# Performance work log

Measured on AMD Instinct MI355X. Metric: run time of the kernel, lower is better.

The kernel has to match this reference:

```python
import jax, jax.numpy as jnp
import numpy as np

N = 10000      # nodes
S = 4          # num_samples (walks per node)
L = 8          # walk length
F_IN = 128     # in_features == out_features (required by SelfSupervise fc)
H = 128        # out_features (GRU hidden)
ORIG = 64      # original_features
SUB = 100      # self-supervision subsample


def _gru(x, h0, Wih, Whh, bih, bhh):
    """Single-layer unidirectional GRU. x: (L, *batch, F); h0: (*batch, H)."""
    def step(hprev, xt):
        gi = xt @ Wih.T + bih            # (*batch, 3H)
        gh = hprev @ Whh.T + bhh
        ir, iz, inn = jnp.split(gi, 3, axis=-1)
        hr, hz, hn = jnp.split(gh, 3, axis=-1)
        r = jax.nn.sigmoid(ir + hr)
        z = jax.nn.sigmoid(iz + hz)
        n = jnp.tanh(inn + r * hn)
        hnew = (1.0 - z) * n + z * hprev
        return hnew, hnew
    hT, ys = jax.lax.scan(step, h0, x)
    return ys, hT                         # ys: (L, *batch, H), hT: (*batch, H)


def setup_inputs() -> dict:
    key = jax.random.key(0)
    ks = jax.random.split(key, 14)
    s = 0.1  # weight scale for numerical sanity
    return {
        "h":     jax.random.normal(ks[0], (N, F_IN), jnp.float32),
        "y0":    jax.random.uniform(ks[1], (N, ORIG), jnp.float32),  # binary-ish targets in [0,1]
        "Wih_w": s * jax.random.normal(ks[2], (3 * H, L), jnp.float32),
        "Whh_w": s * jax.random.normal(ks[3], (3 * H, H), jnp.float32),
        "bih_w": s * jax.random.normal(ks[4], (3 * H,), jnp.float32),
        "bhh_w": s * jax.random.normal(ks[5], (3 * H,), jnp.float32),
        "Wih":   s * jax.random.normal(ks[6], (3 * H, F_IN + H), jnp.float32),
        "Whh":   s * jax.random.normal(ks[7], (3 * H, H), jnp.float32),
        "bih":   s * jax.random.normal(ks[8], (3 * H,), jnp.float32),
        "bhh":   s * jax.random.normal(ks[9], (3 * H,), jnp.float32),
        "W_ss":  s * jax.random.normal(ks[10], (ORIG, F_IN), jnp.float32),
        "b_ss":  s * jax.random.normal(ks[11], (ORIG,), jnp.float32),
        "walks": jax.random.randint(ks[12], (S, N, L), 0, N),
        "idxs":  jax.random.randint(ks[13], (SUB,), 0, N),
    }


def reference(h, y0, Wih_w, Whh_w, bih_w, bhh_w, Wih, Whh, bih, bhh, W_ss, b_ss, walks, idxs):
    # uniqueness: index of first occurrence of each node within its walk, in [0, L)
    uniq = jnp.argmax(walks[..., :, None] == walks[..., None, :], axis=-1)  # (S, N, L)
    walks_f = jnp.flip(walks, axis=-1)
    uniq_f = jnp.flip(uniq, axis=-1)
    u1h = jax.nn.one_hot(uniq_f, L, dtype=h.dtype)          # (S, N, L, L)

    hw = jnp.take(h, walks_f, axis=0)                       # (S, N, L, F_IN) gather

    h0 = jnp.zeros((S, N, H), dtype=h.dtype)
    x_walk = jnp.moveaxis(u1h, -2, 0)                       # (L, S, N, L)
    y_walk, h_walk = _gru(x_walk, h0, Wih_w, Whh_w, bih_w, bhh_w)  # (L,S,N,H), (S,N,H)
    # torch: h_walk.mean(0, keepdim=True) over layer dim of size 1 -> identity

    x_main = jnp.concatenate([jnp.moveaxis(hw, -2, 0), y_walk], axis=-1)  # (L, S, N, F_IN+H)
    y_seq, hT = _gru(x_main, h_walk, Wih, Whh, bih, bhh)    # (L,S,N,H), (S,N,H)
    y = jnp.moveaxis(y_seq, 0, -2)                          # (S, N, L, H)

    # self-supervision: subsample nodes, next-step BCE
    y_t = jnp.take(y0, walks_f, axis=0)[:, idxs, 1:, :]     # (S, SUB, L-1, ORIG)
    y_hat = y[:, idxs, :-1, :] @ W_ss.T + b_ss              # (S, SUB, L-1, ORIG)
    pos_w = 1.0 / jnp.mean(y_t)
    loss = jnp.mean(pos_w * y_t * jax.nn.softplus(-y_hat)
                    + (1.0 - y_t) * jax.nn.softplus(y_hat))

    # torch: h.mean(0) over layer dim of size 1 -> hT; activation = Identity; dropout = eval
    return hT, loss
```

## Files before the change

kernel.cpp:

```cpp
#include <hip/hip_runtime.h>
#include <math.h>

#define NN    10000
#define SSS   4
#define LL    8
#define HH    128
#define NSEQ  40000
#define SUBN  100
#define ORIGF 64
#define MA    48
#define NS    3
#define TA    512

typedef unsigned short u16;
typedef short bf16x8 __attribute__((ext_vector_type(8)));
typedef float f32x4 __attribute__((ext_vector_type(4)));

#define L2E 1.4426950408889634f

#define WL_OFF    0
#define BWRZ_OFF  6144
#define BWIN_OFF  7168
#define BWHN_OFF  7680
#define BMRZ_OFF  8192
#define BMIN_OFF  9216
#define BMHN_OFF  9728
#define HB_OFF    10240
#define HBBUF     2176
#define HB_STR    136
#define HB_SSTR   (2*HBBUF)
#define XB_OFF    36352
#define XB_STR    136
#define XB_SSTR   (128*136)
#define SWF_OFF   140800
#define SUF_OFF   142336
#define SCNT_OFF  143872
#define SANY_OFF  144064
#define LDS_TOTAL 144128

#define WB_BYTE_OFF 64
#define W_HHW_N 49152
#define W_HH_N  49152
#define W_IH_N  98304
#define W_TOTAL (W_HHW_N + W_HH_N + W_IH_N)
#define WS_NEED ((size_t)WB_BYTE_OFF + (size_t)W_TOTAL * 2 + (size_t)NN * HH * 2)

__device__ __forceinline__ float bf2f(u16 u) {
  return __uint_as_float(((unsigned)u) << 16);
}
__device__ __forceinline__ u16 f2bf(float f) {
  unsigned u = __float_as_uint(f);
  u += 0x7fffu + ((u >> 16) & 1u);
  return (u16)(u >> 16);
}
__device__ __forceinline__ bf16x8 pack8(float4 v0, float4 v1) {
  bf16x8 r;
  r[0] = (short)f2bf(v0.x); r[1] = (short)f2bf(v0.y);
  r[2] = (short)f2bf(v0.z); r[3] = (short)f2bf(v0.w);
  r[4] = (short)f2bf(v1.x); r[5] = (short)f2bf(v1.y);
  r[6] = (short)f2bf(v1.z); r[7] = (short)f2bf(v1.w);
  return r;
}
__device__ __forceinline__ float sig2_(float xs) {
  return __builtin_amdgcn_rcpf(1.f + __builtin_amdgcn_exp2f(-xs));
}
__device__ __forceinline__ float tanh2_(float xs) {
  return 1.f - 2.f * __builtin_amdgcn_rcpf(__builtin_amdgcn_exp2f(xs) + 1.f);
}
__device__ __forceinline__ float softplusf_(float x) {
  return fmaxf(x, 0.f) + log1pf(__expf(-fabsf(x)));
}

__global__ void k_zero(float* ws) {
  if (threadIdx.x < 4) ws[threadIdx.x] = 0.f;
}

__global__ void k_prep(const float* __restrict__ whhw, const float* __restrict__ whh,
                       const float* __restrict__ wih, float* __restrict__ ws) {
  const int i = blockIdx.x * 256 + threadIdx.x;
  u16* wb = (u16*)((char*)ws + WB_BYTE_OFF);
  if (i < W_HHW_N) {
    const int row = i >> 7;
    wb[i] = f2bf(whhw[i] * ((row < 256) ? L2E : 2.f * L2E));
  } else if (i < W_HHW_N + W_HH_N) {
    const int j = i - W_HHW_N, row = j >> 7;
    wb[i] = f2bf(whh[j] * ((row < 256) ? L2E : 2.f * L2E));
  } else {
    const int j = i - W_HHW_N - W_HH_N, row = j >> 8;
    wb[i] = f2bf(wih[j] * ((row < 256) ? L2E : 2.f * L2E));
  }
}

__global__ void k_prep_h(const float* __restrict__ h, float* __restrict__ ws) {
  const int i = blockIdx.x * 256 + threadIdx.x;
  u16* hb16 = (u16*)((char*)ws + WB_BYTE_OFF) + W_TOTAL;
  hb16[i] = f2bf(h[i]);
}

template<bool BF>
__global__ __launch_bounds__(TA, 2) void k_rum(
    const float* __restrict__ hfeat, const float* __restrict__ y0,
    const float* __restrict__ WihW,  const float* __restrict__ bihW,
    const float* __restrict__ bhhW,
    const float* __restrict__ bih,   const float* __restrict__ bhh,
    const float* __restrict__ W_ss,  const float* __restrict__ b_ss,
    const int* __restrict__ walks,   const int* __restrict__ idxs,
    float* __restrict__ out, float* __restrict__ ws)
{
  extern __shared__ char sm[];
  u16*   WLb  = (u16*)(sm + WL_OFF);
  float* bwrz = (float*)(sm + BWRZ_OFF);
  float* bwin = (float*)(sm + BWIN_OFF);
  float* bwhn = (float*)(sm + BWHN_OFF);
  float* bmrz = (float*)(sm + BMRZ_OFF);
  float* bmin = (float*)(sm + BMIN_OFF);
  float* bmhn = (float*)(sm + BMHN_OFF);
  u16*   hb   = (u16*)(sm + HB_OFF);
  u16*   xb   = (u16*)(sm + XB_OFF);
  int*   swf  = (int*)(sm + SWF_OFF);
  int*   suf  = (int*)(sm + SUF_OFF);
  int*   scnt = (int*)(sm + SCNT_OFF);
  int*   sany = (int*)(sm + SANY_OFF);

  const u16* wb     = (const u16*)((const char*)ws + WB_BYTE_OFF);
  const u16* whhw_b = wb;
  const u16* whh_b  = wb + W_HHW_N;
  const u16* wih_b  = wb + W_HHW_N + W_HH_N;
  const u16* hf16   = wb + W_TOTAL;

  const int tid = threadIdx.x;
  const int lane = tid & 63, c = lane & 15, qd = lane >> 4;
  const int wv = tid >> 6;
  const int i0 = wv * 16 + c;
  const int q0 = blockIdx.x * MA;

  if (tid < MA) {
    const int m = tid;
    scnt[m] = 0;
    const int q = q0 + m;
    if (q < NSEQ) {
      int w[LL];
      #pragma unroll
      for (int l = 0; l < LL; ++l) w[l] = walks[q * LL + l];
      #pragma unroll
      for (int l = 0; l < LL; ++l) {
        int u = l;
        #pragma unroll
        for (int l2 = LL - 1; l2 >= 0; --l2) if (w[l2] == w[l]) u = l2;
        swf[m * LL + (LL - 1 - l)] = w[l];
        suf[m * LL + (LL - 1 - l)] = u;
      }
    } else {
      #pragma unroll
      for (int l = 0; l < LL; ++l) { swf[m * LL + l] = 0; suf[m * LL + l] = 0; }
    }
  }
  if (tid == 0) *sany = 0;
  for (int idx = tid; idx < 3072; idx += TA)
    WLb[idx] = f2bf(WihW[idx] * ((idx < 2048) ? L2E : 2.f * L2E));
  if (tid < 256) {
    bwrz[tid] = (bihW[tid] + bhhW[tid]) * L2E;
    bmrz[tid] = (bih[tid] + bhh[tid]) * L2E;
  }
  if (tid < 128) {
    bwin[tid] = 2.f * L2E * bihW[256 + tid]; bwhn[tid] = 2.f * L2E * bhhW[256 + tid];
    bmin[tid] = 2.f * L2E * bih[256 + tid];  bmhn[tid] = 2.f * L2E * bhh[256 + tid];
  }
  __syncthreads();

  for (int p = tid; p < MA * SUBN; p += TA) {
    const int m = p / SUBN, i = p % SUBN;
    if ((q0 + m) < NSEQ && idxs[i] == (q0 + m) % NN) {
      atomicAdd(&scnt[m], 1); *sany = 1;
    }
  }

  const float bw1 = bwrz[i0], bw2 = bwrz[HH + i0], bw3 = bwin[i0], bw4 = bwhn[i0];
  const float bm1 = bmrz[i0], bm2 = bmrz[HH + i0], bm3 = bmin[i0], bm4 = bmhn[i0];

  float hreg[NS][4];
  #pragma unroll
  for (int s = 0; s < NS; ++s)
    #pragma unroll
    for (int r2 = 0; r2 < 4; ++r2) hreg[s][r2] = 0.f;

  {
    bf16x8 BA[3][4];
    #pragma unroll
    for (int tl = 0; tl < 3; ++tl) {
      const int row = (tl * 8 + wv) * 16 + c;
      #pragma unroll
      for (int k = 0; k < 4; ++k)
        BA[tl][k] = *(const bf16x8*)(whhw_b + row * HH + k * 32 + qd * 8);
    }
    #pragma unroll 2
    for (int t = 0; t < LL; ++t) {
      #pragma unroll
      for (int s = 0; s < NS; ++s) {
        f32x4 D[3];
        #pragma unroll
        for (int tl = 0; tl < 3; ++tl) D[tl] = (f32x4){0.f, 0.f, 0.f, 0.f};
        if (t > 0) {
          const u16* hbc = hb + s * HB_SSTR + (t & 1) * HBBUF;
          bf16x8 a[4];
          #pragma unroll
          for (int k = 0; k < 4; ++k)
            a[k] = *(const bf16x8*)(hbc + c * HB_STR + k * 32 + qd * 8);
          #pragma unroll
          for (int tl = 0; tl < 3; ++tl) {
            f32x4 d = D[tl];
            #pragma unroll
            for (int k = 0; k < 4; ++k)
              d = __builtin_amdgcn_mfma_f32_16x16x32_bf16(a[k], BA[tl][k], d, 0, 0, 0);
            D[tl] = d;
          }
        }
        u16* hbn = hb + s * HB_SSTR + ((t + 1) & 1) * HBBUF;
        u16* xbs = xb + s * XB_SSTR;
        #pragma unroll
        for (int reg = 0; reg < 4; ++reg) {
          const int ml = qd * 4 + reg;
          const int u = suf[(s * 16 + ml) * LL + t];
          const float r = sig2_(bf2f(WLb[i0 * LL + u]) + D[0][reg] + bw1);
          const float z = sig2_(bf2f(WLb[(HH + i0) * LL + u]) + D[1][reg] + bw2);
          const float n = tanh2_(bf2f(WLb[(2 * HH + i0) * LL + u]) + bw3
                                 + r * (D[2][reg] + bw4));
          const float hn = n + z * (hreg[s][reg] - n);
          hreg[s][reg] = hn;
          const u16 hv = f2bf(hn);
          hbn[ml * HB_STR + i0] = hv;
          xbs[(t * 16 + ml) * XB_STR + i0] = hv;
        }
      }
      __syncthreads();
    }
  }

  const bool anyf = (*sany != 0);

  bf16x8 BW[3][8], BC[3][4];
  #pragma unroll
  for (int tl = 0; tl < 3; ++tl) {
    const int row = (tl * 8 + wv) * 16 + c;
    #pragma unroll
    for (int kk = 0; kk < 8; ++kk)
      BW[tl][kk] = *(const bf16x8*)(wih_b + row * 256 + kk * 32 + qd * 8);
    #pragma unroll
    for (int k = 0; k < 4; ++k)
      BC[tl][k] = *(const bf16x8*)(whh_b + row * HH + k * 32 + qd * 8);
  }

  float pAcc = 0.f, pBcc = 0.f, pScc = 0.f;

  #pragma unroll 2
  for (int t = 0; t < LL; ++t) {
    #pragma unroll
    for (int s = 0; s < NS; ++s) {
      const int node = swf[(s * 16 + c) * LL + t];
      bf16x8 ah[4];
      if constexpr (BF) {
        const u16* hp = hf16 + (size_t)node * HH + qd * 8;
        #pragma unroll
        for (int k = 0; k < 4; ++k) ah[k] = *(const bf16x8*)(hp + k * 32);
      } else {
        const float* hp = hfeat + (size_t)node * HH + qd * 8;
        #pragma unroll
        for (int k = 0; k < 4; ++k)
          ah[k] = pack8(*(const float4*)(hp + k * 32),
                        *(const float4*)(hp + k * 32 + 4));
      }
      const u16* xbs = xb + s * XB_SSTR;
      bf16x8 ay[4];
      #pragma unroll
      for (int k = 0; k < 4; ++k)
        ay[k] = *(const bf16x8*)(xbs + (t * 16 + c) * XB_STR + k * 32 + qd * 8);
      const u16* hbc = hb + s * HB_SSTR + (t & 1) * HBBUF;
      bf16x8 a[4];
      #pragma unroll
      for (int k = 0; k < 4; ++k)
        a[k] = *(const bf16x8*)(hbc + c * HB_STR + k * 32 + qd * 8);

      f32x4 Drz[2], Dnr, Dni;
      #pragma unroll
      for (int tl = 0; tl < 2; ++tl) {
        f32x4 d = {0.f, 0.f, 0.f, 0.f};
        #pragma unroll
        for (int k = 0; k < 4; ++k)
          d = __builtin_amdgcn_mfma_f32_16x16x32_bf16(a[k], BC[tl][k], d, 0, 0, 0);
        #pragma unroll
        for (int k = 0; k < 4; ++k)
          d = __builtin_amdgcn_mfma_f32_16x16x32_bf16(ah[k], BW[tl][k], d, 0, 0, 0);
        #pragma unroll
        for (int k = 0; k < 4; ++k)
          d = __builtin_amdgcn_mfma_f32_16x16x32_bf16(ay[k], BW[tl][4 + k], d, 0, 0, 0);
        Drz[tl] = d;
      }
      {
        f32x4 dr = {0.f, 0.f, 0.f, 0.f}, di = {0.f, 0.f, 0.f, 0.f};
        #pragma unroll
        for (int k = 0; k < 4; ++k)
          dr = __builtin_amdgcn_mfma_f32_16x16x32_bf16(a[k], BC[2][k], dr, 0, 0, 0);
        #pragma unroll
        for (int k = 0; k < 4; ++k)
          di = __builtin_amdgcn_mfma_f32_16x16x32_bf16(ah[k], BW[2][k], di, 0, 0, 0);
        #pragma unroll
        for (int k = 0; k < 4; ++k)
          di = __builtin_amdgcn_mfma_f32_16x16x32_bf16(ay[k], BW[2][4 + k], di, 0, 0, 0);
        Dnr = dr; Dni = di;
      }
      u16* hbn = hb + s * HB_SSTR + ((t + 1) & 1) * HBBUF;
      #pragma unroll
      for (int reg = 0; reg < 4; ++reg) {
        const int ml = qd * 4 + reg;
        const float r = sig2_(Drz[0][reg] + bm1);
        const float z = sig2_(Drz[1][reg] + bm2);
        const float n = tanh2_(Dni[reg] + bm3 + r * (Dnr[reg] + bm4));
        const float hn = n + z * (hreg[s][reg] - n);
        hreg[s][reg] = hn;
        hbn[ml * HB_STR + i0] = f2bf(hn);
      }
    }

    if (t < LL - 1 && anyf) {
      __syncthreads();
      for (int idx = tid; idx < MA * ORIGF; idx += TA) {
        const int m = idx >> 6, o = idx & 63;
        const int cnt = scnt[m];
        if (cnt > 0) {
          const u16* hrow = hb + (m >> 4) * HB_SSTR + ((t + 1) & 1) * HBBUF
                          + (m & 15) * HB_STR;
          const float* wr = W_ss + o * HH;
          float acc = b_ss[o];
          #pragma unroll 1
          for (int kc = 0; kc < HH; kc += 8) {
            const float4 wa = *(const float4*)(wr + kc);
            const float4 wb4 = *(const float4*)(wr + kc + 4);
            const bf16x8 xv = *(const bf16x8*)(hrow + kc);
            acc = fmaf(wa.x, bf2f((u16)xv[0]), acc);
            acc = fmaf(wa.y, bf2f((u16)xv[1]), acc);
            acc = fmaf(wa.z, bf2f((u16)xv[2]), acc);
            acc = fmaf(wa.w, bf2f((u16)xv[3]), acc);
            acc = fmaf(wb4.x, bf2f((u16)xv[4]), acc);
            acc = fmaf(wb4.y, bf2f((u16)xv[5]), acc);
            acc = fmaf(wb4.z, bf2f((u16)xv[6]), acc);
            acc = fmaf(wb4.w, bf2f((u16)xv[7]), acc);
          }
          const float fc = (float)cnt;
          const float yt = y0[(size_t)swf[m * LL + t + 1] * ORIGF + o];
          pAcc += fc * yt * softplusf_(-acc);
          pBcc += fc * (1.f - yt) * softplusf_(acc);
          pScc += fc * yt;
        }
      }
    }
    __syncthreads();
  }

  #pragma unroll
  for (int s = 0; s < NS; ++s)
    #pragma unroll
    for (int reg = 0; reg < 4; ++reg) {
      const int q = q0 + s * 16 + qd * 4 + reg;
      if (q < NSEQ) out[(size_t)q * HH + i0] = hreg[s][reg];
    }

  if (anyf) {
    float* red = (float*)(sm + WL_OFF);
    red[tid] = pAcc; red[TA + tid] = pBcc; red[2 * TA + tid] = pScc;
    __syncthreads();
    if (wv == 0) {
      float a = 0.f, b = 0.f, s = 0.f;
      for (int k2 = lane; k2 < TA; k2 += 64) {
        a += red[k2]; b += red[TA + k2]; s += red[2 * TA + k2];
      }
      #pragma unroll
      for (int off = 32; off > 0; off >>= 1) {
        a += __shfl_down(a, off); b += __shfl_down(b, off); s += __shfl_down(s, off);
      }
      if (lane == 0) {
        atomicAdd(&ws[1], a); atomicAdd(&ws[2], b); atomicAdd(&ws[3], s);
      }
    }
  }
}

__global__ void k_final(const float* __restrict__ ws, float* __restrict__ out) {
  if (threadIdx.x == 0) {
    const float cnt = (float)(SSS * SUBN * (LL - 1) * ORIGF);
    const float pos_w = cnt / ws[3];
    const float loss = (pos_w * ws[1] + ws[2]) / cnt;
    out[NSEQ * HH] = loss;
  }
}

extern "C" void kernel_launch(void* const* d_in, const int* in_sizes, int n_in,
                              void* d_out, int out_size, void* d_ws, size_t ws_size,
                              hipStream_t stream) {
  const float* hfeat = (const float*)d_in[0];
  const float* y0    = (const float*)d_in[1];
  const float* Wih_w = (const float*)d_in[2];
  const float* Whh_w = (const float*)d_in[3];
  const float* bih_w = (const float*)d_in[4];
  const float* bhh_w = (const float*)d_in[5];
  const float* Wih   = (const float*)d_in[6];
  const float* Whh   = (const float*)d_in[7];
  const float* bih   = (const float*)d_in[8];
  const float* bhh   = (const float*)d_in[9];
  const float* W_ss  = (const float*)d_in[10];
  const float* b_ss  = (const float*)d_in[11];
  const int* walks = (const int*)d_in[12];
  const int* idxs  = (const int*)d_in[13];
  float* out = (float*)d_out;
  float* ws = (float*)d_ws;

  const bool bf = (ws_size >= WS_NEED);

  (void)hipFuncSetAttribute((const void*)k_rum<true>,
                            hipFuncAttributeMaxDynamicSharedMemorySize, LDS_TOTAL);
  (void)hipFuncSetAttribute((const void*)k_rum<false>,
                            hipFuncAttributeMaxDynamicSharedMemorySize, LDS_TOTAL);

  k_zero<<<1, 64, 0, stream>>>(ws);
  k_prep<<<W_TOTAL / 256, 256, 0, stream>>>(Whh_w, Whh, Wih, ws);
  if (bf) k_prep_h<<<(NN * HH) / 256, 256, 0, stream>>>(hfeat, ws);

  const int grid = (NSEQ + MA - 1) / MA;
  if (bf)
    k_rum<true><<<grid, TA, LDS_TOTAL, stream>>>(hfeat, y0, Wih_w, bih_w, bhh_w,
                                                 bih, bhh, W_ss, b_ss,
                                                 walks, idxs, out, ws);
  else
    k_rum<false><<<grid, TA, LDS_TOTAL, stream>>>(hfeat, y0, Wih_w, bih_w, bhh_w,
                                                  bih, bhh, W_ss, b_ss,
                                                  walks, idxs, out, ws);

  k_final<<<1, 64, 0, stream>>>(ws, out);
}
```

Measured before the change: 391.1 us.

## Prefetch gathered node features into LDS asynchronously and XOR-swizzle LDS tiles

Replaces per-step direct global gathers of bf16 node features with global_load_lds prefetches into a double-buffered LDS region, issued one timestep ahead so the gather latency overlaps with the MFMA work of the current step. It also removes the row padding in the hidden-state and walk-output LDS buffers and uses an XOR swizzle on 16-byte chunks to avoid bank conflicts, which frees LDS for the prefetch buffers. Total LDS use grows, and correctness depends on the async LDS writes being visible at the existing barriers.

```diff
diff --git a/kernel.cpp b/kernel.cpp
--- a/kernel.cpp
+++ b/kernel.cpp
@@ -26,17 +26,20 @@
 #define BMIN_OFF  9216
 #define BMHN_OFF  9728
 #define HB_OFF    10240
-#define HBBUF     2176
-#define HB_STR    136
-#define HB_SSTR   (2*HBBUF)
-#define XB_OFF    36352
-#define XB_STR    136
-#define XB_SSTR   (128*136)
-#define SWF_OFF   140800
-#define SUF_OFF   142336
-#define SCNT_OFF  143872
-#define SANY_OFF  144064
-#define LDS_TOTAL 144128
+#define HB_STR    128
+#define HBBUF     2048
+#define HB_SSTR   4096
+#define XB_OFF    34816
+#define XB_STR    128
+#define XB_SSTR   16384
+#define PF_OFF    133120
+#define PF_DB     6144
+#define PF_SSTR   2048
+#define SWF_OFF   157696
+#define SUF_OFF   159232
+#define SCNT_OFF  160768
+#define SANY_OFF  160960
+#define LDS_TOTAL 161024
 
 #define WB_BYTE_OFF 64
 #define W_HHW_N 49152
@@ -69,6 +72,11 @@
 }
 __device__ __forceinline__ float softplusf_(float x) {
   return fmaxf(x, 0.f) + log1pf(__expf(-fabsf(x)));
+}
+typedef __attribute__((address_space(3))) unsigned int lds_u32;
+typedef const __attribute__((address_space(1))) unsigned int glb_u32;
+__device__ __forceinline__ void gload_lds16(const void* g, void* l) {
+  __builtin_amdgcn_global_load_lds((glb_u32*)g, (lds_u32*)l, 16, 0, 0);
 }
 
 __global__ void k_zero(float* ws) {
@@ -117,6 +125,7 @@
   float* bmhn = (float*)(sm + BMHN_OFF);
   u16*   hb   = (u16*)(sm + HB_OFF);
   u16*   xb   = (u16*)(sm + XB_OFF);
+  u16*   pf   = (u16*)(sm + PF_OFF);
   int*   swf  = (int*)(sm + SWF_OFF);
   int*   suf  = (int*)(sm + SUF_OFF);
   int*   scnt = (int*)(sm + SCNT_OFF);
@@ -168,6 +177,22 @@
   }
   __syncthreads();
 
+  if constexpr (BF) {
+    const int rr = lane >> 4, s16 = lane & 15;
+    #pragma unroll
+    for (int s = 0; s < NS; ++s)
+      #pragma unroll
+      for (int ii = 0; ii < 4; ++ii) {
+        const int q = s * 4 + ii;
+        if (q == wv || q == wv + 8) {
+          const int row = ii * 4 + rr;
+          const int node = swf[(s * 16 + row) * LL + 0];
+          gload_lds16(hf16 + (size_t)node * HH + ((s16 ^ row) << 3),
+                      pf + s * PF_SSTR + ii * 512);
+        }
+      }
+  }
+
   for (int p = tid; p < MA * SUBN; p += TA) {
     const int m = p / SUBN, i = p % SUBN;
     if ((q0 + m) < NSEQ && idxs[i] == (q0 + m) % NN) {
@@ -205,7 +230,7 @@
           bf16x8 a[4];
           #pragma unroll
           for (int k = 0; k < 4; ++k)
-            a[k] = *(const bf16x8*)(hbc + c * HB_STR + k * 32 + qd * 8);
+            a[k] = *(const bf16x8*)(hbc + c * HB_STR + (((4 * k + qd) ^ c) << 3));
           #pragma unroll
           for (int tl = 0; tl < 3; ++tl) {
             f32x4 d = D[tl];
@@ -228,8 +253,9 @@
           const float hn = n + z * (hreg[s][reg] - n);
           hreg[s][reg] = hn;
           const u16 hv = f2bf(hn);
-          hbn[ml * HB_STR + i0] = hv;
-          xbs[(t * 16 + ml) * XB_STR + i0] = hv;
+          const int slot = (((i0 >> 3) ^ ml) << 3) + (i0 & 7);
+          hbn[ml * HB_STR + slot] = hv;
+          xbs[(t * 16 + ml) * XB_STR + slot] = hv;
         }
       }
       __syncthreads();
@@ -254,31 +280,49 @@
 
   #pragma unroll 2
   for (int t = 0; t < LL; ++t) {
+    if constexpr (BF) {
+      if (t < LL - 1) {
+        const int rr = lane >> 4, s16 = lane & 15;
+        #pragma unroll
+        for (int s = 0; s < NS; ++s)
+          #pragma unroll
+          for (int ii = 0; ii < 4; ++ii) {
+            const int q = s * 4 + ii;
+            if (q == wv || q == wv + 8) {
+              const int row = ii * 4 + rr;
+              const int node = swf[(s * 16 + row) * LL + (t + 1)];
+              gload_lds16(hf16 + (size_t)node * HH + ((s16 ^ row) << 3),
+                          pf + ((t + 1) & 1) * PF_DB + s * PF_SSTR + ii * 512);
+            }
+          }
+      }
+    }
     #pragma unroll
     for (int s = 0; s < NS; ++s) {
-      const int node = swf[(s * 16 + c) * LL + t];
       bf16x8 ah[4];
       if constexpr (BF) {
-        const u16* hp = hf16 + (size_t)node * HH + qd * 8;
-        #pragma unroll
-        for (int k = 0; k < 4; ++k) ah[k] = *(const bf16x8*)(hp + k * 32);
+        const u16* pfs = pf + (t & 1) * PF_DB + s * PF_SSTR;
+        #pragma unroll
+        for (int k = 0; k < 4; ++k)
+          ah[k] = *(const bf16x8*)(pfs + c * HB_STR + (((4 * k + qd) ^ c) << 3));
       } else {
+        const int node = swf[(s * 16 + c) * LL + t];
         const float* hp = hfeat + (size_t)node * HH + qd * 8;
         #pragma unroll
         for (int k = 0; k < 4; ++k)
           ah[k] = pack8(*(const float4*)(hp + k * 32),
                         *(const float4*)(hp + k * 32 + 4));
       }
-      const u16* xbs = xb + s * XB_SSTR;
+      const u16* xbs = xb + s * XB_SSTR + t * 16 * XB_STR;
       bf16x8 ay[4];
       #pragma unroll
       for (int k = 0; k < 4; ++k)
-        ay[k] = *(const bf16x8*)(xbs + (t * 16 + c) * XB_STR + k * 32 + qd * 8);
+        ay[k] = *(const bf16x8*)(xbs + c * XB_STR + (((4 * k + qd) ^ c) << 3));
       const u16* hbc = hb + s * HB_SSTR + (t & 1) * HBBUF;
       bf16x8 a[4];
       #pragma unroll
       for (int k = 0; k < 4; ++k)
-        a[k] = *(const bf16x8*)(hbc + c * HB_STR + k * 32 + qd * 8);
+        a[k] = *(const bf16x8*)(hbc + c * HB_STR + (((4 * k + qd) ^ c) << 3));
 
       f32x4 Drz[2], Dnr, Dni;
       #pragma unroll
@@ -317,7 +361,7 @@
         const float n = tanh2_(Dni[reg] + bm3 + r * (Dnr[reg] + bm4));
         const float hn = n + z * (hreg[s][reg] - n);
         hreg[s][reg] = hn;
-        hbn[ml * HB_STR + i0] = f2bf(hn);
+        hbn[ml * HB_STR + (((i0 >> 3) ^ ml) << 3) + (i0 & 7)] = f2bf(hn);
       }
     }
 
@@ -327,15 +371,16 @@
         const int m = idx >> 6, o = idx & 63;
         const int cnt = scnt[m];
         if (cnt > 0) {
+          const int ml = m & 15;
           const u16* hrow = hb + (m >> 4) * HB_SSTR + ((t + 1) & 1) * HBBUF
-                          + (m & 15) * HB_STR;
+                          + ml * HB_STR;
           const float* wr = W_ss + o * HH;
           float acc = b_ss[o];
           #pragma unroll 1
-          for (int kc = 0; kc < HH; kc += 8) {
-            const float4 wa = *(const float4*)(wr + kc);
-            const float4 wb4 = *(const float4*)(wr + kc + 4);
-            const bf16x8 xv = *(const bf16x8*)(hrow + kc);
+          for (int kc8 = 0; kc8 < 16; ++kc8) {
+            const float4 wa = *(const float4*)(wr + kc8 * 8);
+            const float4 wb4 = *(const float4*)(wr + kc8 * 8 + 4);
+            const bf16x8 xv = *(const bf16x8*)(hrow + ((kc8 ^ ml) << 3));
             acc = fmaf(wa.x, bf2f((u16)xv[0]), acc);
             acc = fmaf(wa.y, bf2f((u16)xv[1]), acc);
             acc = fmaf(wa.z, bf2f((u16)xv[2]), acc);
```

Measured after the change: 674.3 us. +72.4%, slower.
